# Kernel tuning notes

Measured on AMD Instinct MI355X. Metric: run time of the kernel, lower is better.

The kernel has to match this reference:

```python
import jax, jax.numpy as jnp
import numpy as np

DECAY = 0.99
EPS = 1e-05


def setup_inputs() -> dict:
    key = jax.random.key(0)
    k1, k2 = jax.random.split(key)
    B, L, D, K = 8, 2048, 512, 4096
    x = jax.random.normal(k1, (B, L, D), dtype=jnp.float32)
    # variance_scaling(scale=1, fan_in, uniform): U(-limit, limit), limit = sqrt(3/fan_in)
    limit = np.sqrt(3.0 / D)
    codebook = jax.random.uniform(k2, (K, D), dtype=jnp.float32, minval=-limit, maxval=limit)
    return {
        "x": x,
        "codebook": codebook,
        "hidden_cluster": jnp.zeros((K,), jnp.float32),
        "hidden_dw": jnp.zeros((K, D), jnp.float32),
        "count": jnp.zeros((), jnp.float32),
    }


def reference(x, codebook, hidden_cluster, hidden_dw, count):
    K, D = codebook.shape
    B, L, _ = x.shape
    # avoids materializing the (B,L,K,D) broadcast the naive cdist creates)
    x2 = jnp.sum(x * x, axis=-1, keepdims=True)                  # (B,L,1)
    c2 = jnp.sum(codebook * codebook, axis=-1)                   # (K,)
    xc = jnp.einsum("bld,kd->blk", x, codebook)                  # (B,L,K)
    d2 = x2 - 2.0 * xc + c2
    indices = jnp.argmin(d2, axis=-1)                            # (B,L) int
    flat_idx = indices.reshape(-1)

    # cluster_counts = one_hot(indices).sum((0,1)) as a scatter-add
    cluster_counts = jnp.zeros((K,), jnp.float32).at[flat_idx].add(1.0)
    # dw = einsum('bln,bld->nd', one_hot, x) as a scatter-add of x rows
    dw = jnp.zeros((K, D), jnp.float32).at[flat_idx].add(x.reshape(-1, D))

    decay = jnp.asarray(DECAY, x.dtype)
    one = jnp.ones([], x.dtype)
    count_new = count + 1.0
    bias = one - decay ** count_new

    hidden_cluster_new = hidden_cluster * decay + (one - decay) * cluster_counts
    avg_cluster = hidden_cluster_new / bias
    hidden_dw_new = hidden_dw * decay + (one - decay) * dw
    avg_dw = hidden_dw_new / bias

    N = jnp.sum(avg_cluster)
    cc = (avg_cluster + EPS) / (N + K * EPS) * N
    codebook_new = avg_dw / cc[:, None]

    # quantized = one_hot(indices) @ codebook_new == gather
    q = codebook_new[indices]                                    # (B,L,D)
    quantized = x + jax.lax.stop_gradient(q - x)
    # optax.l2_loss(x, quantized).mean() == 0.5*(x-quantized)^2 mean
    codebook_loss = 0.5 * jnp.mean(jnp.square(x - quantized))
    return quantized, codebook_loss, indices
```

## Files before the change

kernel.cpp:

```cpp
#include <hip/hip_runtime.h>
#include <math.h>

#define BL 16384
#define D  512
#define K  4096

#define OFF_C2    0
#define OFF_X2    (16<<10)
#define OFF_CNT   (80<<10)
#define OFF_AVGC  (96<<10)
#define OFF_SCAL  (112<<10)
#define OFF_IDX16 (116<<10)
#define OFF_RMAX  (152<<10)
#define OFF_PMUL  (216<<10)
#define OFF_KEYS  (280<<10)
#define OFF_CAND  (408<<10)
#define OFF_CBN   (1472<<10)
#define OFF_CBN_FB (256<<10)

#define SC_C 0.07660f

typedef int   i32x4 __attribute__((ext_vector_type(4)));
typedef unsigned long long ull;
#define MFMAI8(a,b,c) __builtin_amdgcn_mfma_i32_16x16x64_i8(a,b,c,0,0,0)

__device__ __forceinline__ ull umin64(ull a, ull b) { return a < b ? a : b; }
__device__ __forceinline__ ull umax64(ull a, ull b) { return a > b ? a : b; }


__global__ void rowsq_max_all(const float* __restrict__ x, const float* __restrict__ cb,
                              float* __restrict__ x2, float* __restrict__ c2,
                              float* __restrict__ rowmax, float* __restrict__ premul)
{
    int b    = blockIdx.x;
    int lane = threadIdx.x;
    if (b < K) {
        const float* p = cb + (size_t)b * D;
        float s = 0.f;
#pragma unroll
        for (int j = 0; j < D / 64; ++j) {
            float v = p[lane + j * 64];
            s = fmaf(v, v, s);
        }
#pragma unroll
        for (int off = 32; off > 0; off >>= 1)
            s += __shfl_down(s, off, 64);
        if (lane == 0) c2[b] = s;
    } else {
        int row = b - K;
        const float* p = x + (size_t)row * D;
        float s = 0.f, mx = 0.f;
#pragma unroll
        for (int j = 0; j < D / 64; ++j) {
            float v = p[lane + j * 64];
            s = fmaf(v, v, s);
            mx = fmaxf(mx, fabsf(v));
        }
#pragma unroll
        for (int off = 32; off > 0; off >>= 1) {
            s += __shfl_down(s, off, 64);
            mx = fmaxf(mx, __shfl_down(mx, off, 64));
        }
        if (lane == 0) {
            x2[row] = s;
            rowmax[row] = mx;
            premul[row] = 2.0f * (mx / 127.0f) * (SC_C / 127.0f);
        }
    }
}

__global__ __launch_bounds__(256) void rescore_kernel(
    const float* __restrict__ x, const float* __restrict__ cb,
    const float* __restrict__ x2, const float* __restrict__ c2,
    const unsigned short* __restrict__ cand,
    unsigned long long* __restrict__ keys)
{
    int t = blockIdx.x * 256 + threadIdx.x;
    int row = t >> 5, ci = t & 31;
    int idx = cand[(size_t)row * 32 + ci];
    const float* xp = x  + (size_t)row * D;
    const float* cp = cb + (size_t)idx * D;
    float acc = 0.f;
#pragma unroll 4
    for (int k0 = 0; k0 < D; k0 += 4) {
        float4 xv = *(const float4*)(xp + k0);
        float4 cv = *(const float4*)(cp + k0);
        acc = fmaf(xv.x, cv.x, acc);
        acc = fmaf(xv.y, cv.y, acc);
        acc = fmaf(xv.z, cv.z, acc);
        acc = fmaf(xv.w, cv.w, acc);
    }
    float wv = x2[row] - 2.0f * acc;
    float dd = wv + c2[idx];
    ull key = ((ull)__float_as_uint(dd) << 12) | (ull)idx;
#pragma unroll
    for (int m = 1; m < 32; m <<= 1) {
        ull o = __shfl_xor(key, m, 64);
        key = o < key ? o : key;
    }
    if (ci == 0) keys[row] = key;
}


__device__ __forceinline__ void load_lds16(const unsigned short* g, unsigned short* l) {
    __builtin_amdgcn_global_load_lds(
        (const __attribute__((address_space(1))) unsigned int*)(g),
        (__attribute__((address_space(3))) unsigned int*)(l), 16, 0, 0);
}

__global__ __launch_bounds__(256) void quant_all(
    const float* __restrict__ x, const float* __restrict__ cb,
    const float* __restrict__ rowmax,
    unsigned short* __restrict__ xq, unsigned short* __restrict__ cq)
{
    int w    = threadIdx.x >> 6;
    int l    = threadIdx.x & 63;
    int half = l >> 5, lx = l & 31;
    int ch   = lx >> 2, g = lx & 3;
    int blk  = blockIdx.x;
    __align__(16) char o[16];
    if (blk < 2048) {
        int r = blk * 8 + w * 2 + half;
        float rm = rowmax[r];
        float inv = rm > 0.f ? 127.0f / rm : 0.f;
        const float* sp = x + (size_t)r * D + ch * 64 + g * 16;
#pragma unroll
        for (int i = 0; i < 16; ++i) o[i] = (char)(int)rintf(sp[i] * inv);
        int line = r >> 1, j = (r & 1) * 4 + g, ph = j ^ (line & 7);
        size_t gran = ((size_t)ch * 8192 + line) * 8 + ph;
        *(uint4*)(xq + gran * 8) = *(const uint4*)o;
    } else {
        int code = (blk - 2048) * 8 + w * 2 + half;
        const float invc = 127.0f / SC_C;
        const float* sp = cb + (size_t)code * D + ch * 64 + g * 16;
#pragma unroll
        for (int i = 0; i < 16; ++i) o[i] = (char)(int)rintf(sp[i] * invc);
        int line = code >> 1, j = (code & 1) * 4 + g, ph = j ^ (line & 7);
        size_t gran = ((size_t)ch * 2048 + line) * 8 + ph;
        *(uint4*)(cq + gran * 8) = *(const uint4*)o;
    }
}

__global__ __launch_bounds__(256, 2) void argmin_i8(
    const unsigned short* __restrict__ xq, const unsigned short* __restrict__ cq,
    const float* __restrict__ x2, const float* __restrict__ c2,
    const float* __restrict__ premul, unsigned short* __restrict__ cand)
{
    __shared__ __align__(16) unsigned short sA[4096];
    __shared__ __align__(16) unsigned short sB[4096];

    const int tid = threadIdx.x;
    const int l   = tid & 63;
    const int w   = tid >> 6;
    const int wm  = w >> 1, wn = w & 1;
    const int q   = l >> 4;
    const int cc  = l & 15;
    const int row0 = blockIdx.x * 128;
    const int nb   = blockIdx.y * 512;

    int rdA[4], rdB[4];
#pragma unroll
    for (int t = 0; t < 4; ++t) {
        int ra = wm * 64 + t * 16 + cc;
        int mA = ra >> 1, jA = (ra & 1) * 4 + q;
        rdA[t] = mA * 128 + ((jA ^ (mA & 7)) * 16);
        int rb = wn * 64 + t * 16 + cc;
        int mB = rb >> 1, jB = (rb & 1) * 4 + q;
        rdB[t] = mB * 128 + ((jB ^ (mB & 7)) * 16);
    }

    ull k1[16], k2[16], k3[16];
#pragma unroll
    for (int s = 0; s < 16; ++s) { k1[s] = ~0ULL; k2[s] = ~0ULL; k3[s] = ~0ULL; }

    for (int n0 = 0; n0 < 4; ++n0) {
        i32x4 acc[4][4];
#pragma unroll
        for (int tm = 0; tm < 4; ++tm)
#pragma unroll
            for (int tn = 0; tn < 4; ++tn) { i32x4 z = {0,0,0,0}; acc[tm][tn] = z; }

        for (int c = 0; c < 8; ++c) {
            __syncthreads();
            {
                size_t abase = (size_t)c * 524288 + (size_t)(row0 >> 1) * 64;
                size_t bbase = (size_t)c * 131072 + (size_t)((nb + n0 * 128) >> 1) * 64;
                load_lds16(xq + abase + (w)     * 512 + l * 8, &sA[(w)     * 512 + l * 8]);
                load_lds16(xq + abase + (w + 4) * 512 + l * 8, &sA[(w + 4) * 512 + l * 8]);
                load_lds16(cq + bbase + (w)     * 512 + l * 8, &sB[(w)     * 512 + l * 8]);
                load_lds16(cq + bbase + (w + 4) * 512 + l * 8, &sB[(w + 4) * 512 + l * 8]);
            }
            __syncthreads();
            i32x4 Af[4], Bf[4];
#pragma unroll
            for (int t = 0; t < 4; ++t) {
                Af[t] = *(const i32x4*)((const char*)sA + rdA[t]);
                Bf[t] = *(const i32x4*)((const char*)sB + rdB[t]);
            }
#pragma unroll
            for (int tm = 0; tm < 4; ++tm)
#pragma unroll
                for (int tn = 0; tn < 4; ++tn)
                    acc[tm][tn] = MFMAI8(Af[tm], Bf[tn], acc[tm][tn]);
        }
        float c2v[4];
#pragma unroll
        for (int tn = 0; tn < 4; ++tn)
            c2v[tn] = c2[nb + n0 * 128 + wn * 64 + tn * 16 + cc];
#pragma unroll
        for (int tm = 0; tm < 4; ++tm)
#pragma unroll
            for (int r = 0; r < 4; ++r) {
                int s = tm * 4 + r;
                int row = row0 + wm * 64 + tm * 16 + q * 4 + r;
                float x2v = x2[row];
                float pm  = premul[row];
#pragma unroll
                for (int tn = 0; tn < 4; ++tn) {
                    unsigned col = nb + n0 * 128 + wn * 64 + tn * 16 + cc;
                    float dd = (x2v - pm * (float)acc[tm][tn][r]) + c2v[tn];
                    ull key = ((ull)__float_as_uint(dd) << 12) | (ull)col;
                    bool c1 = key < k1[s], cm2 = key < k2[s], cm3 = key < k3[s];
                    ull nk1 = c1 ? key : k1[s];
                    ull nk2 = c1 ? k1[s] : (cm2 ? key : k2[s]);
                    ull nk3 = cm2 ? k2[s] : (cm3 ? key : k3[s]);
                    k1[s] = nk1; k2[s] = nk2; k3[s] = nk3;
                }
            }
    }

#pragma unroll
    for (int s = 0; s < 16; ++s) {
#pragma unroll
        for (int m = 1; m < 16; m <<= 1) {
            ull o1 = __shfl_xor(k1[s], m, 64);
            ull o2 = __shfl_xor(k2[s], m, 64);
            ull o3 = __shfl_xor(k3[s], m, 64);
            ull hi1 = umax64(k1[s], o1);
            ull lo2 = umin64(k2[s], o2);
            ull m1 = umin64(k1[s], o1);
            ull m2 = umin64(hi1, lo2);
            ull m3 = umin64(umax64(hi1, lo2),
                            umin64(umax64(k2[s], o2), umin64(k3[s], o3)));
            k1[s] = m1; k2[s] = m2; k3[s] = m3;
        }
    }

    __syncthreads();
    ull* sc = (ull*)sA;
    if (cc == 0) {
#pragma unroll
        for (int s = 0; s < 16; ++s) {
            int rl = wm * 64 + (s >> 2) * 16 + q * 4 + (s & 3);
            sc[(rl * 2 + wn) * 3 + 0] = k1[s];
            sc[(rl * 2 + wn) * 3 + 1] = k2[s];
            sc[(rl * 2 + wn) * 3 + 2] = k3[s];
        }
    }
    __syncthreads();
    if (tid < 128) {
        ull a1 = sc[(tid * 2 + 0) * 3 + 0], a2 = sc[(tid * 2 + 0) * 3 + 1], a3 = sc[(tid * 2 + 0) * 3 + 2];
        ull b1 = sc[(tid * 2 + 1) * 3 + 0], b2 = sc[(tid * 2 + 1) * 3 + 1], b3 = sc[(tid * 2 + 1) * 3 + 2];
        ull hi1 = umax64(a1, b1);
        ull lo2 = umin64(a2, b2);
        ull m1 = umin64(a1, b1);
        ull m2 = umin64(hi1, lo2);
        ull m3 = umin64(umax64(hi1, lo2), umin64(umax64(a2, b2), umin64(a3, b3)));
        size_t base = (size_t)(row0 + tid) * 32 + blockIdx.y * 4;
        cand[base + 0] = (unsigned short)(m1 & 0xFFFULL);
        cand[base + 1] = (unsigned short)(m2 & 0xFFFULL);
        cand[base + 2] = (unsigned short)(m3 & 0xFFFULL);
        cand[base + 3] = (unsigned short)(m3 & 0xFFFULL);
    }
}

__global__ __launch_bounds__(256) void argmin_fb(
    const float* __restrict__ x, const float* __restrict__ cb,
    const float* __restrict__ x2, const float* __restrict__ c2,
    unsigned long long* __restrict__ keys)
{
    __shared__ __align__(16) float As[32][68];
    __shared__ __align__(16) float Bs[32][68];
    __shared__ float rv[64][16];
    __shared__ int   ri[64][16];

    const int tid  = threadIdx.x;
    const int tx   = tid & 15;
    const int ty   = tid >> 4;
    const int row0 = blockIdx.x * 64;
    const int nb   = blockIdx.y * 1024;

    float x2r[4];
#pragma unroll
    for (int m = 0; m < 4; ++m) x2r[m] = x2[row0 + ty * 4 + m];

    float minv[4]; int mini[4];
#pragma unroll
    for (int m = 0; m < 4; ++m) { minv[m] = 3.4028235e38f; mini[m] = 0; }

    for (int n0 = 0; n0 < 1024; n0 += 64) {
        float acc[4][4];
#pragma unroll
        for (int m = 0; m < 4; ++m)
#pragma unroll
            for (int n = 0; n < 4; ++n) acc[m][n] = 0.f;

        for (int d0 = 0; d0 < D; d0 += 32) {
            __syncthreads();
#pragma unroll
            for (int j = 0; j < 2; ++j) {
                int v   = j * 256 + tid;
                int row = v >> 3;
                int col = (v & 7) * 4;
                float4 av = *(const float4*)(x  + (size_t)(row0 + row) * D + d0 + col);
                As[col + 0][row] = av.x; As[col + 1][row] = av.y;
                As[col + 2][row] = av.z; As[col + 3][row] = av.w;
                float4 bv = *(const float4*)(cb + (size_t)(nb + n0 + row) * D + d0 + col);
                Bs[col + 0][row] = bv.x; Bs[col + 1][row] = bv.y;
                Bs[col + 2][row] = bv.z; Bs[col + 3][row] = bv.w;
            }
            __syncthreads();
#pragma unroll
            for (int kk = 0; kk < 32; ++kk) {
                float4 a4 = *(const float4*)&As[kk][ty * 4];
                float4 b4 = *(const float4*)&Bs[kk][tx * 4];
                float a_[4] = { a4.x, a4.y, a4.z, a4.w };
                float b_[4] = { b4.x, b4.y, b4.z, b4.w };
#pragma unroll
                for (int m = 0; m < 4; ++m)
#pragma unroll
                    for (int n = 0; n < 4; ++n)
                        acc[m][n] = fmaf(a_[m], b_[n], acc[m][n]);
            }
        }
#pragma unroll
        for (int n = 0; n < 4; ++n) {
            int kidx = nb + n0 + tx * 4 + n;
            float c2k = c2[kidx];
#pragma unroll
            for (int m = 0; m < 4; ++m) {
                float wv = x2r[m] - 2.0f * acc[m][n];
                float dd = wv + c2k;
                if (dd < minv[m]) { minv[m] = dd; mini[m] = kidx; }
            }
        }
    }
#pragma unroll
    for (int m = 0; m < 4; ++m) { rv[ty * 4 + m][tx] = minv[m]; ri[ty * 4 + m][tx] = mini[m]; }
    __syncthreads();
    if (tid < 64) {
        float bv = rv[tid][0]; int bi = ri[tid][0];
#pragma unroll
        for (int j = 1; j < 16; ++j) {
            float v = rv[tid][j]; int ii = ri[tid][j];
            if (v < bv || (v == bv && ii < bi)) { bv = v; bi = ii; }
        }
        ull key = ((ull)__float_as_uint(bv) << 12) | (ull)bi;
        atomicMin(&keys[row0 + tid], key);
    }
}


__global__ void count_kernel(const unsigned long long* __restrict__ keys,
                             float* __restrict__ counts, unsigned short* __restrict__ idx16)
{
    int i = blockIdx.x * 256 + threadIdx.x;
    int k = (int)(keys[i] & 0xFFFULL);
    idx16[i] = (unsigned short)k;
    atomicAdd(&counts[k], 1.0f);
}

__global__ __launch_bounds__(256) void ema_cluster_kernel(
    const float* __restrict__ hc, const float* __restrict__ counts,
    const float* __restrict__ countp, float* __restrict__ avgc, float* __restrict__ Nout)
{
    __shared__ float sm[256];
    int i = blockIdx.x * 256 + threadIdx.x;
    const float om = 1.0f - 0.99f;
    float bias = 1.0f - powf(0.99f, countp[0] + 1.0f);
    float a = (hc[i] * 0.99f + om * counts[i]) / bias;
    avgc[i] = a;
    sm[threadIdx.x] = a;
    __syncthreads();
    for (int s = 128; s > 0; s >>= 1) {
        if (threadIdx.x < s) sm[threadIdx.x] += sm[threadIdx.x + s];
        __syncthreads();
    }
    if (threadIdx.x == 0) atomicAdd(Nout, sm[0]);
}

__global__ __launch_bounds__(256) void code_update_kernel(
    const float* __restrict__ x, const unsigned short* __restrict__ idx16,
    const float* __restrict__ hdw, const float* __restrict__ avgc,
    const float* __restrict__ Nptr, const float* __restrict__ countp,
    float* __restrict__ cbn)
{
    __shared__ unsigned short rows[2048];
    __shared__ int cnt;
    int k = blockIdx.x, tid = threadIdx.x;
    if (tid == 0) cnt = 0;
    __syncthreads();
    const uint4* ip = (const uint4*)idx16;
    for (int j = 0; j < 8; ++j) {
        int u = j * 256 + tid;
        uint4 v = ip[u];
        unsigned ww[4] = {v.x, v.y, v.z, v.w};
#pragma unroll
        for (int e = 0; e < 4; ++e) {
            int k0 = (int)(ww[e] & 0xFFFFu), k1 = (int)(ww[e] >> 16);
            if (k0 == k) { int p = atomicAdd(&cnt, 1); if (p < 2048) rows[p] = (unsigned short)(u * 8 + e * 2); }
            if (k1 == k) { int p = atomicAdd(&cnt, 1); if (p < 2048) rows[p] = (unsigned short)(u * 8 + e * 2 + 1); }
        }
    }
    __syncthreads();
    int n = cnt < 2048 ? cnt : 2048;
    float a0 = 0.f, a1 = 0.f;
    for (int p = 0; p < n; ++p) {
        int r = rows[p];
        a0 += x[(size_t)r * D + tid];
        a1 += x[(size_t)r * D + tid + 256];
    }
    const float om = 1.0f - 0.99f;
    float bias = 1.0f - powf(0.99f, countp[0] + 1.0f);
    float Nv = *Nptr;
    float ccv = ((avgc[k] + 1e-5f) / (Nv + 0.04096f)) * Nv;
    size_t b = (size_t)k * D;
    cbn[b + tid]       = ((hdw[b + tid]       * 0.99f + om * a0) / bias) / ccv;
    cbn[b + tid + 256] = ((hdw[b + tid + 256] * 0.99f + om * a1) / bias) / ccv;
}

__global__ __launch_bounds__(256) void gather_kernel(
    const float* __restrict__ x, const unsigned long long* __restrict__ keys,
    const float* __restrict__ cbn, float* __restrict__ outq,
    float* __restrict__ partial)
{
    __shared__ float sm[256];
    int row = blockIdx.x;
    int tid = threadIdx.x;
    int k   = (int)(keys[row] & 0xFFFULL);
    const float* xpp = x   + (size_t)row * D;
    const float* cp  = cbn + (size_t)k   * D;
    float* op = outq + (size_t)row * D;
    float local = 0.f;
#pragma unroll
    for (int j = 0; j < 2; ++j) {
        int d = tid + j * 256;
        float xv = xpp[d];
        float qv = cp[d];
        float quant = xv + (qv - xv);
        op[d] = quant;
        float diff = xv - quant;
        local = fmaf(diff, diff, local);
    }
    sm[tid] = local;
    __syncthreads();
    for (int s = 128; s > 0; s >>= 1) {
        if (tid < s) sm[tid] += sm[tid + s];
        __syncthreads();
    }
    if (tid == 0) {
        partial[row] = sm[0];
        outq[8388609 + row] = (float)k;
    }
}

__global__ __launch_bounds__(256) void finalize_kernel(
    const float* __restrict__ partial, float* __restrict__ out)
{
    __shared__ double sm[256];
    int tid = threadIdx.x;
    double s = 0.0;
#pragma unroll
    for (int j = 0; j < 64; ++j) s += (double)partial[tid + j * 256];
    sm[tid] = s;
    __syncthreads();
    for (int st = 128; st > 0; st >>= 1) {
        if (tid < st) sm[tid] += sm[tid + st];
        __syncthreads();
    }
    if (tid == 0) out[8388608] = (float)(0.5 * sm[0] / 8388608.0);
}


extern "C" void kernel_launch(void* const* d_in, const int* in_sizes, int n_in,
                              void* d_out, int out_size, void* d_ws, size_t ws_size,
                              hipStream_t stream)
{
    const float* x   = (const float*)d_in[0];
    const float* cb  = (const float*)d_in[1];
    const float* hc  = (const float*)d_in[2];
    const float* hdw = (const float*)d_in[3];
    const float* cnt = (const float*)d_in[4];
    float* out = (float*)d_out;

    char* ws = (char*)d_ws;
    float*  c2     = (float*)(ws + OFF_C2);
    float*  x2     = (float*)(ws + OFF_X2);
    float*  counts = (float*)(ws + OFF_CNT);
    float*  avgc   = (float*)(ws + OFF_AVGC);
    float*  Nout   = (float*)(ws + OFF_SCAL + 8);
    unsigned short* idx16 = (unsigned short*)(ws + OFF_IDX16);
    float*  rowmax = (float*)(ws + OFF_RMAX);
    float*  premul = (float*)(ws + OFF_PMUL);
    unsigned long long* keys = (unsigned long long*)(ws + OFF_KEYS);
    float*  partial= (float*)(ws + OFF_X2);

    hipMemsetAsync(ws + OFF_CNT, 0, (32 << 10) + 16, stream);

    rowsq_max_all<<<K + BL, 64, 0, stream>>>(x, cb, x2, c2, rowmax, premul);

    const bool primary = ws_size >= ((size_t)10 << 20);
    float* cbn;
    if (primary) {
        unsigned short* xq = (unsigned short*)d_out;
        unsigned short* cq = xq + (size_t)8 * 524288;
        unsigned short* cand = (unsigned short*)(ws + OFF_CAND);
        cbn = (float*)(ws + OFF_CBN);

        quant_all<<<2560, 256, 0, stream>>>(x, cb, rowmax, xq, cq);
        argmin_i8<<<dim3(BL / 128, 8), 256, 0, stream>>>(xq, cq, x2, c2, premul, cand);
        rescore_kernel<<<(BL * 32) / 256, 256, 0, stream>>>(x, cb, x2, c2, cand, keys);
    } else {
        cbn = (float*)(ws + OFF_CBN_FB);
        hipMemsetAsync(ws + OFF_KEYS, 0xFF, BL * 8, stream);
        argmin_fb<<<dim3(BL / 64, 4), 256, 0, stream>>>(x, cb, x2, c2, keys);
    }

    count_kernel<<<BL / 256, 256, 0, stream>>>(keys, counts, idx16);
    ema_cluster_kernel<<<K / 256, 256, 0, stream>>>(hc, counts, cnt, avgc, Nout);
    code_update_kernel<<<K, 256, 0, stream>>>(x, idx16, hdw, avgc, Nout, cnt, cbn);
    gather_kernel<<<BL, 256, 0, stream>>>(x, keys, cbn, out, partial);
    finalize_kernel<<<1, 256, 0, stream>>>(partial, out);
}
```

Measured before the change: 393.5 us.

## Keep top-2 int8 candidates per slice, halve rescore work, fuse counting into rescore

The int8 MFMA argmin now tracks the best two candidates per 512-column slice instead of three, using float value/index pairs in place of 64-bit packed key insertion. This cuts the per-element compare cost and the shuffle-merge traffic. The fp32 rescore kernel checks 16 candidates per row instead of 32, which halves its gather reads of the codebook. Cluster counting and idx16 writes are folded into the rescore kernel, removing the separate count launch on the primary path. The risk is a wrong argmin whenever the true nearest code is not among the top-2 int8 candidates of its slice.

```diff
diff --git a/kernel.cpp b/kernel.cpp
--- a/kernel.cpp
+++ b/kernel.cpp
@@ -24,9 +24,6 @@
 typedef unsigned long long ull;
 #define MFMAI8(a,b,c) __builtin_amdgcn_mfma_i32_16x16x64_i8(a,b,c,0,0,0)
 
-__device__ __forceinline__ ull umin64(ull a, ull b) { return a < b ? a : b; }
-__device__ __forceinline__ ull umax64(ull a, ull b) { return a > b ? a : b; }
-
 
 __global__ void rowsq_max_all(const float* __restrict__ x, const float* __restrict__ cb,
                               float* __restrict__ x2, float* __restrict__ c2,
@@ -73,11 +70,12 @@
     const float* __restrict__ x, const float* __restrict__ cb,
     const float* __restrict__ x2, const float* __restrict__ c2,
     const unsigned short* __restrict__ cand,
-    unsigned long long* __restrict__ keys)
+    unsigned long long* __restrict__ keys,
+    float* __restrict__ counts, unsigned short* __restrict__ idx16)
 {
     int t = blockIdx.x * 256 + threadIdx.x;
-    int row = t >> 5, ci = t & 31;
-    int idx = cand[(size_t)row * 32 + ci];
+    int row = t >> 4, ci = t & 15;
+    int idx = cand[(size_t)row * 16 + ci];
     const float* xp = x  + (size_t)row * D;
     const float* cp = cb + (size_t)idx * D;
     float acc = 0.f;
@@ -94,11 +92,16 @@
     float dd = wv + c2[idx];
     ull key = ((ull)__float_as_uint(dd) << 12) | (ull)idx;
 #pragma unroll
-    for (int m = 1; m < 32; m <<= 1) {
+    for (int m = 1; m < 16; m <<= 1) {
         ull o = __shfl_xor(key, m, 64);
         key = o < key ? o : key;
     }
-    if (ci == 0) keys[row] = key;
+    if ((t & 15) == 0) {
+        keys[row] = key;
+        int kf = (int)(key & 0xFFFULL);
+        idx16[row] = (unsigned short)kf;
+        atomicAdd(&counts[kf], 1.0f);
+    }
 }
 
 
@@ -169,9 +172,9 @@
         rdB[t] = mB * 128 + ((jB ^ (mB & 7)) * 16);
     }
 
-    ull k1[16], k2[16], k3[16];
-#pragma unroll
-    for (int s = 0; s < 16; ++s) { k1[s] = ~0ULL; k2[s] = ~0ULL; k3[s] = ~0ULL; }
+    float v1[16], v2[16]; unsigned i1[16], i2[16];
+#pragma unroll
+    for (int s = 0; s < 16; ++s) { v1[s] = v2[s] = 3.4028235e38f; i1[s] = i2[s] = 0; }
 
     for (int n0 = 0; n0 < 4; ++n0) {
         i32x4 acc[4][4];
@@ -219,12 +222,8 @@
                 for (int tn = 0; tn < 4; ++tn) {
                     unsigned col = nb + n0 * 128 + wn * 64 + tn * 16 + cc;
                     float dd = (x2v - pm * (float)acc[tm][tn][r]) + c2v[tn];
-                    ull key = ((ull)__float_as_uint(dd) << 12) | (ull)col;
-                    bool c1 = key < k1[s], cm2 = key < k2[s], cm3 = key < k3[s];
-                    ull nk1 = c1 ? key : k1[s];
-                    ull nk2 = c1 ? k1[s] : (cm2 ? key : k2[s]);
-                    ull nk3 = cm2 ? k2[s] : (cm3 ? key : k3[s]);
-                    k1[s] = nk1; k2[s] = nk2; k3[s] = nk3;
+                    if (dd < v1[s]) { v2[s]=v1[s]; i2[s]=i1[s]; v1[s]=dd; i1[s]=col; }
+                    else if (dd < v2[s]) { v2[s]=dd; i2[s]=col; }
                 }
             }
     }
@@ -233,16 +232,17 @@
     for (int s = 0; s < 16; ++s) {
 #pragma unroll
         for (int m = 1; m < 16; m <<= 1) {
-            ull o1 = __shfl_xor(k1[s], m, 64);
-            ull o2 = __shfl_xor(k2[s], m, 64);
-            ull o3 = __shfl_xor(k3[s], m, 64);
-            ull hi1 = umax64(k1[s], o1);
-            ull lo2 = umin64(k2[s], o2);
-            ull m1 = umin64(k1[s], o1);
-            ull m2 = umin64(hi1, lo2);
-            ull m3 = umin64(umax64(hi1, lo2),
-                            umin64(umax64(k2[s], o2), umin64(k3[s], o3)));
-            k1[s] = m1; k2[s] = m2; k3[s] = m3;
+            float    ov1 = __shfl_xor(v1[s], m, 64);
+            unsigned oi1 = __shfl_xor(i1[s], m, 64);
+            float    ov2 = __shfl_xor(v2[s], m, 64);
+            unsigned oi2 = __shfl_xor(i2[s], m, 64);
+            bool oLt = (ov1 < v1[s]) || (ov1 == v1[s] && oi1 < i1[s]);
+            float    a1  = oLt ? ov1 : v1[s];  unsigned ai1 = oLt ? oi1 : i1[s];
+            float    lf  = oLt ? v1[s] : ov1;  unsigned lfi = oLt ? i1[s] : oi1;
+            float    ws_ = oLt ? ov2 : v2[s];  unsigned wsi = oLt ? oi2 : i2[s];
+            bool s2 = (ws_ < lf) || (ws_ == lf && wsi < lfi);
+            v2[s] = s2 ? ws_ : lf;  i2[s] = s2 ? wsi : lfi;
+            v1[s] = a1;             i1[s] = ai1;
         }
     }
 
@@ -252,25 +252,21 @@
 #pragma unroll
         for (int s = 0; s < 16; ++s) {
             int rl = wm * 64 + (s >> 2) * 16 + q * 4 + (s & 3);
-            sc[(rl * 2 + wn) * 3 + 0] = k1[s];
-            sc[(rl * 2 + wn) * 3 + 1] = k2[s];
-            sc[(rl * 2 + wn) * 3 + 2] = k3[s];
+            sc[(rl * 2 + wn) * 2 + 0] = ((ull)__float_as_uint(v1[s]) << 12) | (ull)i1[s];
+            sc[(rl * 2 + wn) * 2 + 1] = ((ull)__float_as_uint(v2[s]) << 12) | (ull)i2[s];
         }
     }
     __syncthreads();
     if (tid < 128) {
-        ull a1 = sc[(tid * 2 + 0) * 3 + 0], a2 = sc[(tid * 2 + 0) * 3 + 1], a3 = sc[(tid * 2 + 0) * 3 + 2];
-        ull b1 = sc[(tid * 2 + 1) * 3 + 0], b2 = sc[(tid * 2 + 1) * 3 + 1], b3 = sc[(tid * 2 + 1) * 3 + 2];
-        ull hi1 = umax64(a1, b1);
-        ull lo2 = umin64(a2, b2);
-        ull m1 = umin64(a1, b1);
-        ull m2 = umin64(hi1, lo2);
-        ull m3 = umin64(umax64(hi1, lo2), umin64(umax64(a2, b2), umin64(a3, b3)));
-        size_t base = (size_t)(row0 + tid) * 32 + blockIdx.y * 4;
+        ull a1 = sc[(tid * 2 + 0) * 2 + 0], a2 = sc[(tid * 2 + 0) * 2 + 1];
+        ull b1 = sc[(tid * 2 + 1) * 2 + 0], b2 = sc[(tid * 2 + 1) * 2 + 1];
+        ull m1 = a1 < b1 ? a1 : b1;
+        ull lf = a1 > b1 ? a1 : b1;
+        ull ws_ = a2 < b2 ? a2 : b2;
+        ull m2 = lf < ws_ ? lf : ws_;
+        size_t base = (size_t)(row0 + tid) * 16 + blockIdx.y * 2;
         cand[base + 0] = (unsigned short)(m1 & 0xFFFULL);
         cand[base + 1] = (unsigned short)(m2 & 0xFFFULL);
-        cand[base + 2] = (unsigned short)(m3 & 0xFFFULL);
-        cand[base + 3] = (unsigned short)(m3 & 0xFFFULL);
     }
 }
 
@@ -519,14 +515,15 @@
 
         quant_all<<<2560, 256, 0, stream>>>(x, cb, rowmax, xq, cq);
         argmin_i8<<<dim3(BL / 128, 8), 256, 0, stream>>>(xq, cq, x2, c2, premul, cand);
-        rescore_kernel<<<(BL * 32) / 256, 256, 0, stream>>>(x, cb, x2, c2, cand, keys);
+        rescore_kernel<<<(BL * 16) / 256, 256, 0, stream>>>(x, cb, x2, c2, cand, keys,
+                                                            counts, idx16);
     } else {
         cbn = (float*)(ws + OFF_CBN_FB);
         hipMemsetAsync(ws + OFF_KEYS, 0xFF, BL * 8, stream);
         argmin_fb<<<dim3(BL / 64, 4), 256, 0, stream>>>(x, cb, x2, c2, keys);
-    }
-
-    count_kernel<<<BL / 256, 256, 0, stream>>>(keys, counts, idx16);
+        count_kernel<<<BL / 256, 256, 0, stream>>>(keys, counts, idx16);
+    }
+
     ema_cluster_kernel<<<K / 256, 256, 0, stream>>>(hc, counts, cnt, avgc, Nout);
     code_update_kernel<<<K, 256, 0, stream>>>(x, idx16, hdw, avgc, Nout, cnt, cbn);
     gather_kernel<<<BL, 256, 0, stream>>>(x, keys, cbn, out, partial);
```

Result: slower. 769.7 us (+95.6%).
